# Performance work log

Hardware: AMD Instinct MI355X
Metric: run time of the kernel (lower is better)

## Reference

```python
import jax, jax.numpy as jnp
import numpy as np

N, NFEAT, NHID, NCLASS = 10000, 512, 256, 16
CRF_ITERS = 3


def setup_inputs() -> dict:
    key = jax.random.key(0)
    ks = jax.random.split(key, 10)
    x = jax.random.normal(ks[0], (N, NFEAT), dtype=jnp.float32)
    # sparse-ish adjacency: ~50 neighbors/node, self-loops, row-normalized (GCN style)
    mask = (jax.random.uniform(ks[1], (N, N)) < 0.005).astype(jnp.float32)
    adj = mask + jnp.eye(N, dtype=jnp.float32)
    adj = adj / jnp.sum(adj, axis=1, keepdims=True)
    s1 = 1.0 / np.sqrt(NFEAT)
    s2 = 1.0 / np.sqrt(NHID)
    W1 = jax.random.normal(ks[2], (NFEAT, NHID), dtype=jnp.float32) * s1
    b1 = jnp.zeros((NHID,), dtype=jnp.float32)
    Wq = jax.random.normal(ks[3], (NHID, NHID), dtype=jnp.float32) * s2
    Wk = jax.random.normal(ks[4], (NHID, NHID), dtype=jnp.float32) * s2
    alpha = jnp.float32(1.0)
    beta = jnp.float32(1.0)
    ln_w = jnp.ones((NHID,), dtype=jnp.float32)
    ln_b = jnp.zeros((NHID,), dtype=jnp.float32)
    W2 = jax.random.normal(ks[5], (NHID, NCLASS), dtype=jnp.float32) * s2
    b2 = jnp.zeros((NCLASS,), dtype=jnp.float32)
    return {"x": x, "adj": adj, "W1": W1, "b1": b1, "Wq": Wq, "Wk": Wk,
            "alpha": alpha, "beta": beta, "ln_w": ln_w, "ln_b": ln_b,
            "W2": W2, "b2": b2}


def reference(x, adj, W1, b1, Wq, Wk, alpha, beta, ln_w, ln_b, W2, b2):
    # gc1: adj @ (x W1) + b1, then relu
    h = jax.nn.relu(adj @ (x @ W1) + b1)          # [N, NHID]
    # CRF_Node: adjacency-masked similarity attention, 3 mean-field iterations
    q = h @ Wq
    k = h @ Wk
    scores = (q @ k.T) / jnp.sqrt(jnp.float32(NHID))  # [N, N]
    logits = jnp.where(adj > 0, scores, jnp.float32(-1e9))
    attn = jax.nn.softmax(logits, axis=-1)
    out = h
    for _ in range(CRF_ITERS):
        out = (alpha * h + beta * (attn @ out)) / (alpha + beta)
    # LayerNorm over feature dim
    mu = jnp.mean(out, axis=-1, keepdims=True)
    var = jnp.var(out, axis=-1, keepdims=True)
    out = (out - mu) * jax.lax.rsqrt(var + 1e-5) * ln_w + ln_b
    # dropout: eval mode (identity)
    # gc2 + log_softmax
    y = adj @ (out @ W2) + b2                     # [N, NCLASS]
    return jax.nn.log_softmax(y, axis=-1)
```

## Files before the change

kernel.cpp:

```cpp
#include <hip/hip_runtime.h>
#include <math.h>
#include <float.h>

#define N_NODES 10000
#define NFEAT   512
#define NHID    256
#define NCLASS  16
#define CAP     128

__device__ __forceinline__ float wave_sum(float v) {
#pragma unroll
  for (int o = 32; o > 0; o >>= 1) v += __shfl_down(v, o, 64);
  return v;
}
__device__ __forceinline__ float wave_max(float v) {
#pragma unroll
  for (int o = 32; o > 0; o >>= 1) v = fmaxf(v, __shfl_down(v, o, 64));
  return v;
}

__global__ __launch_bounds__(256) void gemm64(const float* __restrict__ A,
                                              const float* __restrict__ B,
                                              float* __restrict__ C,
                                              int M, int K, int N) {
  __shared__ float As[16][68];
  __shared__ float Bs[16][68];
  const int tid  = threadIdx.x;
  const int row0 = blockIdx.x * 64;
  const int col0 = blockIdx.y * 64;
  const int ty = tid >> 4, tx = tid & 15;
  const int arow = tid >> 2;
  const int akq  = (tid & 3) << 2;
  const int brow = tid >> 4;
  const int bcol = (tid & 15) << 2;

  float acc[4][4] = {};
  for (int k0 = 0; k0 < K; k0 += 16) {
    float4 av = make_float4(0.f, 0.f, 0.f, 0.f);
    const int gr = row0 + arow;
    if (gr < M) av = *(const float4*)&A[(size_t)gr * K + k0 + akq];
    As[akq + 0][arow] = av.x;
    As[akq + 1][arow] = av.y;
    As[akq + 2][arow] = av.z;
    As[akq + 3][arow] = av.w;
    const float4 bv = *(const float4*)&B[(size_t)(k0 + brow) * N + col0 + bcol];
    *(float4*)&Bs[brow][bcol] = bv;
    __syncthreads();
#pragma unroll
    for (int k = 0; k < 16; ++k) {
      const float4 a = *(const float4*)&As[k][ty << 2];
      const float4 b = *(const float4*)&Bs[k][tx << 2];
      acc[0][0] += a.x * b.x; acc[0][1] += a.x * b.y; acc[0][2] += a.x * b.z; acc[0][3] += a.x * b.w;
      acc[1][0] += a.y * b.x; acc[1][1] += a.y * b.y; acc[1][2] += a.y * b.z; acc[1][3] += a.y * b.w;
      acc[2][0] += a.z * b.x; acc[2][1] += a.z * b.y; acc[2][2] += a.z * b.z; acc[2][3] += a.z * b.w;
      acc[3][0] += a.w * b.x; acc[3][1] += a.w * b.y; acc[3][2] += a.w * b.z; acc[3][3] += a.w * b.w;
    }
    __syncthreads();
  }
#pragma unroll
  for (int j = 0; j < 4; ++j) {
    const int gr = row0 + (ty << 2) + j;
    if (gr < M) {
      const float4 o = make_float4(acc[j][0], acc[j][1], acc[j][2], acc[j][3]);
      *(float4*)&C[(size_t)gr * N + col0 + (tx << 2)] = o;
    }
  }
}

__global__ __launch_bounds__(256) void wqwkT(const float* __restrict__ Wq,
                                             const float* __restrict__ Wk,
                                             float* __restrict__ Mm) {
  __shared__ float qr[NHID];
  const int a = blockIdx.x, tid = threadIdx.x;
  qr[tid] = Wq[a * NHID + tid];
  __syncthreads();
  const float* kb = &Wk[(size_t)tid * NHID];
  float acc = 0.f;
#pragma unroll 8
  for (int c = 0; c < NHID; ++c) acc += qr[c] * kb[c];
  Mm[a * NHID + tid] = acc;
}

__global__ __launch_bounds__(256) void scan_build(const float* __restrict__ adj,
                                                  const float* __restrict__ xW1,
                                                  const float* __restrict__ b1,
                                                  int* __restrict__ cols,
                                                  float* __restrict__ vals,
                                                  int* __restrict__ nnz,
                                                  float* __restrict__ h) {
  __shared__ int   lcols[CAP];
  __shared__ float lvals[CAP];
  __shared__ int   scols[CAP];
  __shared__ float svals[CAP];
  __shared__ int   cnt;
  const int row = blockIdx.x, tid = threadIdx.x;
  if (tid == 0) cnt = 0;
  __syncthreads();
  const float4* arow = (const float4*)&adj[(size_t)row * N_NODES];
  for (int v = tid; v < N_NODES / 4; v += 256) {
    const float4 f = arow[v];
    if (f.x != 0.f) { int p = atomicAdd(&cnt, 1); if (p < CAP) { lcols[p] = 4 * v + 0; lvals[p] = f.x; } }
    if (f.y != 0.f) { int p = atomicAdd(&cnt, 1); if (p < CAP) { lcols[p] = 4 * v + 1; lvals[p] = f.y; } }
    if (f.z != 0.f) { int p = atomicAdd(&cnt, 1); if (p < CAP) { lcols[p] = 4 * v + 2; lvals[p] = f.z; } }
    if (f.w != 0.f) { int p = atomicAdd(&cnt, 1); if (p < CAP) { lcols[p] = 4 * v + 3; lvals[p] = f.w; } }
  }
  __syncthreads();
  const int c = min(cnt, CAP);
  int myc = 0; float myv = 0.f; int rank = 0;
  if (tid < c) {
    myc = lcols[tid]; myv = lvals[tid];
    for (int e = 0; e < c; ++e) rank += (lcols[e] < myc);
  }
  __syncthreads();
  if (tid < c) { scols[rank] = myc; svals[rank] = myv; }
  __syncthreads();
  if (tid == 0) nnz[row] = c;
  if (tid < c) {
    cols[(size_t)row * CAP + tid] = scols[tid];
    vals[(size_t)row * CAP + tid] = svals[tid];
  }
  float acc = b1[tid];
  for (int e = 0; e < c; ++e)
    acc += svals[e] * xW1[(size_t)scols[e] * NHID + tid];
  h[(size_t)row * NHID + tid] = fmaxf(acc, 0.f);
}

__global__ __launch_bounds__(256) void attn_crf1(const float* __restrict__ t,
                                                 const float* __restrict__ h,
                                                 const int* __restrict__ cols,
                                                 const int* __restrict__ nnz,
                                                 float* __restrict__ attn,
                                                 float* __restrict__ outn,
                                                 const float* __restrict__ alpha_p,
                                                 const float* __restrict__ beta_p) {
  __shared__ float s[CAP];
  __shared__ int   lcols[CAP];
  __shared__ float lv[CAP];
  __shared__ float red[4], red2[4];
  const int row = blockIdx.x, tid = threadIdx.x;
  const int lane = tid & 63, wv = tid >> 6;
  const int c = nnz[row];
  if (tid < c) lcols[tid] = cols[(size_t)row * CAP + tid];
  const float4 tq = *(const float4*)&t[(size_t)row * NHID + (lane << 2)];
  __syncthreads();
  for (int e = wv; e < c; e += 4) {
    const float4 kq = *(const float4*)&h[(size_t)lcols[e] * NHID + (lane << 2)];
    float p = tq.x * kq.x + tq.y * kq.y + tq.z * kq.z + tq.w * kq.w;
    p = wave_sum(p);
    if (lane == 0) s[e] = p * 0.0625f;
  }
  __syncthreads();
  float m = (tid < c) ? s[tid] : -FLT_MAX;
  m = wave_max(m);
  if (lane == 0) red[wv] = m;
  __syncthreads();
  m = fmaxf(fmaxf(red[0], red[1]), fmaxf(red[2], red[3]));
  const float ev = (tid < c) ? expf(s[tid] - m) : 0.f;
  float sum = wave_sum(ev);
  if (lane == 0) red2[wv] = sum;
  __syncthreads();
  sum = red2[0] + red2[1] + red2[2] + red2[3];
  if (tid < c) {
    const float a = ev / sum;
    attn[(size_t)row * CAP + tid] = a;
    lv[tid] = a;
  }
  __syncthreads();
  float acc = 0.f;
  for (int e = 0; e < c; ++e)
    acc += lv[e] * h[(size_t)lcols[e] * NHID + tid];
  const float a = alpha_p[0], b = beta_p[0];
  outn[(size_t)row * NHID + tid] =
      (a * h[(size_t)row * NHID + tid] + b * acc) / (a + b);
}

__global__ __launch_bounds__(256) void crf_iter(const float* __restrict__ h,
                                                const float* __restrict__ attn,
                                                const int* __restrict__ cols,
                                                const int* __restrict__ nnz,
                                                const float* __restrict__ outp,
                                                float* __restrict__ outn,
                                                const float* __restrict__ alpha_p,
                                                const float* __restrict__ beta_p) {
  __shared__ int   lcols[CAP];
  __shared__ float lv[CAP];
  const int row = blockIdx.x, tid = threadIdx.x;
  const int c = nnz[row];
  if (tid < c) {
    lcols[tid] = cols[(size_t)row * CAP + tid];
    lv[tid]    = attn[(size_t)row * CAP + tid];
  }
  __syncthreads();
  float acc = 0.f;
  for (int e = 0; e < c; ++e)
    acc += lv[e] * outp[(size_t)lcols[e] * NHID + tid];
  const float a = alpha_p[0], b = beta_p[0];
  outn[(size_t)row * NHID + tid] =
      (a * h[(size_t)row * NHID + tid] + b * acc) / (a + b);
}

__global__ __launch_bounds__(256) void crf_ln_w2(const float* __restrict__ h,
                                                 const float* __restrict__ attn,
                                                 const int* __restrict__ cols,
                                                 const int* __restrict__ nnz,
                                                 const float* __restrict__ outp,
                                                 const float* __restrict__ alpha_p,
                                                 const float* __restrict__ beta_p,
                                                 const float* __restrict__ lnw,
                                                 const float* __restrict__ lnb,
                                                 const float* __restrict__ W2,
                                                 float* __restrict__ z) {
  __shared__ int   lcols[CAP];
  __shared__ float lv[CAP];
  __shared__ float r1[4], r2[4], vs[NHID];
  __shared__ float part[16][17];
  const int row = blockIdx.x, tid = threadIdx.x;
  const int lane = tid & 63, wv = tid >> 6;
  const int c = nnz[row];
  if (tid < c) {
    lcols[tid] = cols[(size_t)row * CAP + tid];
    lv[tid]    = attn[(size_t)row * CAP + tid];
  }
  __syncthreads();
  float acc = 0.f;
  for (int e = 0; e < c; ++e)
    acc += lv[e] * outp[(size_t)lcols[e] * NHID + tid];
  const float a = alpha_p[0], b = beta_p[0];
  const float x = (a * h[(size_t)row * NHID + tid] + b * acc) / (a + b);
  float s = wave_sum(x);
  if (lane == 0) r1[wv] = s;
  __syncthreads();
  const float mu = (r1[0] + r1[1] + r1[2] + r1[3]) * (1.f / NHID);
  const float d = x - mu;
  float s2 = wave_sum(d * d);
  if (lane == 0) r2[wv] = s2;
  __syncthreads();
  const float var = (r2[0] + r2[1] + r2[2] + r2[3]) * (1.f / NHID);
  const float v = d * rsqrtf(var + 1e-5f) * lnw[tid] + lnb[tid];
  vs[tid] = v;
  __syncthreads();
  const int cc = tid & 15, g = tid >> 4;
  float p = 0.f;
#pragma unroll
  for (int u = 0; u < 16; ++u)
    p += vs[(g << 4) + u] * W2[((g << 4) + u) * NCLASS + cc];
  part[g][cc] = p;
  __syncthreads();
  if (tid < NCLASS) {
    float q = 0.f;
#pragma unroll
    for (int g2 = 0; g2 < 16; ++g2) q += part[g2][tid];
    z[(size_t)row * NCLASS + tid] = q;
  }
}

__global__ __launch_bounds__(256) void final_k(const float* __restrict__ z,
                                               const float* __restrict__ vals,
                                               const int* __restrict__ cols,
                                               const int* __restrict__ nnz,
                                               const float* __restrict__ b2,
                                               float* __restrict__ out) {
  __shared__ int   lcols[CAP];
  __shared__ float lv[CAP];
  __shared__ float part[16][17];
  __shared__ float ys[16];
  const int row = blockIdx.x, tid = threadIdx.x;
  const int c = nnz[row];
  if (tid < c) {
    lcols[tid] = cols[(size_t)row * CAP + tid];
    lv[tid]    = vals[(size_t)row * CAP + tid];
  }
  __syncthreads();
  const int cc = tid & 15, g = tid >> 4;
  float acc = 0.f;
  for (int e = g; e < c; e += 16)
    acc += lv[e] * z[(size_t)lcols[e] * NCLASS + cc];
  part[g][cc] = acc;
  __syncthreads();
  if (tid < NCLASS) {
    float y = b2[tid];
#pragma unroll
    for (int g2 = 0; g2 < 16; ++g2) y += part[g2][tid];
    ys[tid] = y;
  }
  __syncthreads();
  if (tid < NCLASS) {
    float m = ys[0];
#pragma unroll
    for (int i = 1; i < 16; ++i) m = fmaxf(m, ys[i]);
    float ssum = 0.f;
#pragma unroll
    for (int i = 0; i < 16; ++i) ssum += expf(ys[i] - m);
    out[(size_t)row * NCLASS + tid] = ys[tid] - m - logf(ssum);
  }
}

extern "C" void kernel_launch(void* const* d_in, const int* in_sizes, int n_in,
                              void* d_out, int out_size, void* d_ws, size_t ws_size,
                              hipStream_t stream) {
  const float* x   = (const float*)d_in[0];
  const float* adj = (const float*)d_in[1];
  const float* W1  = (const float*)d_in[2];
  const float* b1  = (const float*)d_in[3];
  const float* Wq  = (const float*)d_in[4];
  const float* Wk  = (const float*)d_in[5];
  const float* al  = (const float*)d_in[6];
  const float* be  = (const float*)d_in[7];
  const float* lnw = (const float*)d_in[8];
  const float* lnb = (const float*)d_in[9];
  const float* W2  = (const float*)d_in[10];
  const float* b2  = (const float*)d_in[11];
  float* out = (float*)d_out;

  char* w = (char*)d_ws;
  size_t off = 0;
  auto alloc = [&](size_t bytes) -> void* {
    void* p = (void*)(w + off);
    off += (bytes + 255) & ~(size_t)255;
    return p;
  };
  float* bufA = (float*)alloc(sizeof(float) * N_NODES * NHID);
  float* h    = (float*)alloc(sizeof(float) * N_NODES * NHID);
  float* outA = (float*)alloc(sizeof(float) * N_NODES * NHID);
  float* Mm   = (float*)alloc(sizeof(float) * NHID * NHID);
  float* z    = (float*)alloc(sizeof(float) * N_NODES * NCLASS);
  int*   cols = (int*)  alloc(sizeof(int)   * N_NODES * CAP);
  float* vals = (float*)alloc(sizeof(float) * N_NODES * CAP);
  float* attn = (float*)alloc(sizeof(float) * N_NODES * CAP);
  int*   nnz  = (int*)  alloc(sizeof(int)   * N_NODES);
  float* xW1  = bufA;
  float* t    = bufA;
  float* outB = bufA;

  const dim3 gg((N_NODES + 63) / 64, NHID / 64);

  gemm64<<<gg, 256, 0, stream>>>(x, W1, xW1, N_NODES, NFEAT, NHID);
  wqwkT<<<NHID, 256, 0, stream>>>(Wq, Wk, Mm);
  scan_build<<<N_NODES, 256, 0, stream>>>(adj, xW1, b1, cols, vals, nnz, h);
  gemm64<<<gg, 256, 0, stream>>>(h, Mm, t, N_NODES, NHID, NHID);
  attn_crf1<<<N_NODES, 256, 0, stream>>>(t, h, cols, nnz, attn, outA, al, be);
  crf_iter<<<N_NODES, 256, 0, stream>>>(h, attn, cols, nnz, outA, outB, al, be);
  crf_ln_w2<<<N_NODES, 256, 0, stream>>>(h, attn, cols, nnz, outB, al, be,
                                         lnw, lnb, W2, z);
  final_k<<<N_NODES, 256, 0, stream>>>(z, vals, cols, nnz, b2, out);
}
```

Baseline: 877.8 us.

## Map one wavefront per row with float4 gathers across sparse CRF kernels

```diff
diff --git a/kernel.cpp b/kernel.cpp
--- a/kernel.cpp
+++ b/kernel.cpp
@@ -8,16 +8,7 @@
 #define NCLASS  16
 #define CAP     128
 
-__device__ __forceinline__ float wave_sum(float v) {
-#pragma unroll
-  for (int o = 32; o > 0; o >>= 1) v += __shfl_down(v, o, 64);
-  return v;
-}
-__device__ __forceinline__ float wave_max(float v) {
-#pragma unroll
-  for (int o = 32; o > 0; o >>= 1) v = fmaxf(v, __shfl_down(v, o, 64));
-  return v;
-}
+typedef float nfloat4 __attribute__((ext_vector_type(4)));
 
 __global__ __launch_bounds__(256) void gemm64(const float* __restrict__ A,
                                               const float* __restrict__ B,
@@ -70,15 +61,19 @@
 __global__ __launch_bounds__(256) void wqwkT(const float* __restrict__ Wq,
                                              const float* __restrict__ Wk,
                                              float* __restrict__ Mm) {
-  __shared__ float qr[NHID];
+  __shared__ float4 qr4[NHID / 4];
   const int a = blockIdx.x, tid = threadIdx.x;
-  qr[tid] = Wq[a * NHID + tid];
-  __syncthreads();
-  const float* kb = &Wk[(size_t)tid * NHID];
+  if (tid < NHID / 4) qr4[tid] = ((const float4*)&Wq[(size_t)a * NHID])[tid];
+  __syncthreads();
+  const float4* kb = (const float4*)&Wk[(size_t)tid * NHID];
   float acc = 0.f;
 #pragma unroll 8
-  for (int c = 0; c < NHID; ++c) acc += qr[c] * kb[c];
-  Mm[a * NHID + tid] = acc;
+  for (int c4 = 0; c4 < NHID / 4; ++c4) {
+    const float4 k4 = kb[c4];
+    const float4 q4 = qr4[c4];
+    acc += q4.x * k4.x + q4.y * k4.y + q4.z * k4.z + q4.w * k4.w;
+  }
+  Mm[(size_t)a * NHID + tid] = acc;
 }
 
 __global__ __launch_bounds__(256) void scan_build(const float* __restrict__ adj,
@@ -88,17 +83,18 @@
                                                   float* __restrict__ vals,
                                                   int* __restrict__ nnz,
                                                   float* __restrict__ h) {
-  __shared__ int   lcols[CAP];
-  __shared__ float lvals[CAP];
-  __shared__ int   scols[CAP];
-  __shared__ float svals[CAP];
-  __shared__ int   cnt;
+  __shared__ int    lcols[CAP];
+  __shared__ float  lvals[CAP];
+  __shared__ int    scols[CAP];
+  __shared__ float  svals[CAP];
+  __shared__ float4 pacc[4][64];
+  __shared__ int    cnt;
   const int row = blockIdx.x, tid = threadIdx.x;
   if (tid == 0) cnt = 0;
   __syncthreads();
-  const float4* arow = (const float4*)&adj[(size_t)row * N_NODES];
+  const nfloat4* arow = (const nfloat4*)&adj[(size_t)row * N_NODES];
   for (int v = tid; v < N_NODES / 4; v += 256) {
-    const float4 f = arow[v];
+    const nfloat4 f = __builtin_nontemporal_load(&arow[v]);
     if (f.x != 0.f) { int p = atomicAdd(&cnt, 1); if (p < CAP) { lcols[p] = 4 * v + 0; lvals[p] = f.x; } }
     if (f.y != 0.f) { int p = atomicAdd(&cnt, 1); if (p < CAP) { lcols[p] = 4 * v + 1; lvals[p] = f.y; } }
     if (f.z != 0.f) { int p = atomicAdd(&cnt, 1); if (p < CAP) { lcols[p] = 4 * v + 2; lvals[p] = f.z; } }
@@ -119,10 +115,26 @@
     cols[(size_t)row * CAP + tid] = scols[tid];
     vals[(size_t)row * CAP + tid] = svals[tid];
   }
-  float acc = b1[tid];
-  for (int e = 0; e < c; ++e)
-    acc += svals[e] * xW1[(size_t)scols[e] * NHID + tid];
-  h[(size_t)row * NHID + tid] = fmaxf(acc, 0.f);
+  const int lane = tid & 63, wv = tid >> 6;
+  float4 acc = make_float4(0.f, 0.f, 0.f, 0.f);
+  for (int e = wv; e < c; e += 4) {
+    const float vv = svals[e];
+    const float4 xv = *(const float4*)&xW1[(size_t)scols[e] * NHID + (lane << 2)];
+    acc.x += vv * xv.x; acc.y += vv * xv.y; acc.z += vv * xv.z; acc.w += vv * xv.w;
+  }
+  pacc[wv][lane] = acc;
+  __syncthreads();
+  if (wv == 0) {
+    const float4 p0 = pacc[0][lane], p1 = pacc[1][lane];
+    const float4 p2 = pacc[2][lane], p3 = pacc[3][lane];
+    const float4 bb = *(const float4*)&b1[lane << 2];
+    float4 r;
+    r.x = fmaxf(bb.x + ((p0.x + p1.x) + (p2.x + p3.x)), 0.f);
+    r.y = fmaxf(bb.y + ((p0.y + p1.y) + (p2.y + p3.y)), 0.f);
+    r.z = fmaxf(bb.z + ((p0.z + p1.z) + (p2.z + p3.z)), 0.f);
+    r.w = fmaxf(bb.w + ((p0.w + p1.w) + (p2.w + p3.w)), 0.f);
+    *(float4*)&h[(size_t)row * NHID + (lane << 2)] = r;
+  }
 }
 
 __global__ __launch_bounds__(256) void attn_crf1(const float* __restrict__ t,
@@ -133,45 +145,70 @@
                                                  float* __restrict__ outn,
                                                  const float* __restrict__ alpha_p,
                                                  const float* __restrict__ beta_p) {
-  __shared__ float s[CAP];
-  __shared__ int   lcols[CAP];
-  __shared__ float lv[CAP];
-  __shared__ float red[4], red2[4];
-  const int row = blockIdx.x, tid = threadIdx.x;
-  const int lane = tid & 63, wv = tid >> 6;
+  __shared__ int   lcols[4][CAP];
+  __shared__ float sv[4][CAP];
+  const int tid = threadIdx.x, lane = tid & 63, wv = tid >> 6;
+  const int row = (blockIdx.x << 2) + wv;
   const int c = nnz[row];
-  if (tid < c) lcols[tid] = cols[(size_t)row * CAP + tid];
-  const float4 tq = *(const float4*)&t[(size_t)row * NHID + (lane << 2)];
-  __syncthreads();
-  for (int e = wv; e < c; e += 4) {
-    const float4 kq = *(const float4*)&h[(size_t)lcols[e] * NHID + (lane << 2)];
-    float p = tq.x * kq.x + tq.y * kq.y + tq.z * kq.z + tq.w * kq.w;
-    p = wave_sum(p);
-    if (lane == 0) s[e] = p * 0.0625f;
-  }
-  __syncthreads();
-  float m = (tid < c) ? s[tid] : -FLT_MAX;
-  m = wave_max(m);
-  if (lane == 0) red[wv] = m;
-  __syncthreads();
-  m = fmaxf(fmaxf(red[0], red[1]), fmaxf(red[2], red[3]));
-  const float ev = (tid < c) ? expf(s[tid] - m) : 0.f;
-  float sum = wave_sum(ev);
-  if (lane == 0) red2[wv] = sum;
-  __syncthreads();
-  sum = red2[0] + red2[1] + red2[2] + red2[3];
-  if (tid < c) {
-    const float a = ev / sum;
-    attn[(size_t)row * CAP + tid] = a;
-    lv[tid] = a;
-  }
-  __syncthreads();
-  float acc = 0.f;
-  for (int e = 0; e < c; ++e)
-    acc += lv[e] * h[(size_t)lcols[e] * NHID + tid];
+  for (int e = lane; e < c; e += 64) lcols[wv][e] = cols[(size_t)row * CAP + e];
+  const int gq = lane >> 4, gl = lane & 15;
+  const float* tp = &t[(size_t)row * NHID + (gl << 2)];
+  const float4 t0 = *(const float4*)&tp[0];
+  const float4 t1 = *(const float4*)&tp[64];
+  const float4 t2 = *(const float4*)&tp[128];
+  const float4 t3 = *(const float4*)&tp[192];
+  for (int e = gq; e < c; e += 4) {
+    const float* hp = &h[(size_t)lcols[wv][e] * NHID + (gl << 2)];
+    const float4 h0 = *(const float4*)&hp[0];
+    const float4 h1 = *(const float4*)&hp[64];
+    const float4 h2 = *(const float4*)&hp[128];
+    const float4 h3 = *(const float4*)&hp[192];
+    float p = t0.x * h0.x + t0.y * h0.y + t0.z * h0.z + t0.w * h0.w
+            + t1.x * h1.x + t1.y * h1.y + t1.z * h1.z + t1.w * h1.w
+            + t2.x * h2.x + t2.y * h2.y + t2.z * h2.z + t2.w * h2.w
+            + t3.x * h3.x + t3.y * h3.y + t3.z * h3.z + t3.w * h3.w;
+    p += __shfl_xor(p, 1, 64);
+    p += __shfl_xor(p, 2, 64);
+    p += __shfl_xor(p, 4, 64);
+    p += __shfl_xor(p, 8, 64);
+    if (gl == 0) sv[wv][e] = p * 0.0625f;
+  }
+  const float s1 = (lane      < c) ? sv[wv][lane]      : -FLT_MAX;
+  const float s2 = (lane + 64 < c) ? sv[wv][lane + 64] : -FLT_MAX;
+  float m = fmaxf(s1, s2);
+#pragma unroll
+  for (int o = 32; o > 0; o >>= 1) m = fmaxf(m, __shfl_xor(m, o, 64));
+  const float e1 = (lane      < c) ? __expf(s1 - m) : 0.f;
+  const float e2 = (lane + 64 < c) ? __expf(s2 - m) : 0.f;
+  float sum = e1 + e2;
+#pragma unroll
+  for (int o = 32; o > 0; o >>= 1) sum += __shfl_xor(sum, o, 64);
+  const float inv = 1.f / sum;
+  if (lane < c) {
+    const float aw = e1 * inv;
+    sv[wv][lane] = aw;
+    attn[(size_t)row * CAP + lane] = aw;
+  }
+  if (lane + 64 < c) {
+    const float aw = e2 * inv;
+    sv[wv][lane + 64] = aw;
+    attn[(size_t)row * CAP + lane + 64] = aw;
+  }
+  float4 acc = make_float4(0.f, 0.f, 0.f, 0.f);
+  for (int e = 0; e < c; ++e) {
+    const float ve = sv[wv][e];
+    const float4 xv = *(const float4*)&h[(size_t)lcols[wv][e] * NHID + (lane << 2)];
+    acc.x += ve * xv.x; acc.y += ve * xv.y; acc.z += ve * xv.z; acc.w += ve * xv.w;
+  }
   const float a = alpha_p[0], b = beta_p[0];
-  outn[(size_t)row * NHID + tid] =
-      (a * h[(size_t)row * NHID + tid] + b * acc) / (a + b);
+  const float i2 = 1.f / (a + b);
+  const float4 hq = *(const float4*)&h[(size_t)row * NHID + (lane << 2)];
+  float4 o4;
+  o4.x = (a * hq.x + b * acc.x) * i2;
+  o4.y = (a * hq.y + b * acc.y) * i2;
+  o4.z = (a * hq.z + b * acc.z) * i2;
+  o4.w = (a * hq.w + b * acc.w) * i2;
+  *(float4*)&outn[(size_t)row * NHID + (lane << 2)] = o4;
 }
 
 __global__ __launch_bounds__(256) void crf_iter(const float* __restrict__ h,
@@ -182,21 +219,39 @@
                                                 float* __restrict__ outn,
                                                 const float* __restrict__ alpha_p,
                                                 const float* __restrict__ beta_p) {
-  __shared__ int   lcols[CAP];
-  __shared__ float lv[CAP];
-  const int row = blockIdx.x, tid = threadIdx.x;
+  __shared__ int   lcols[4][CAP];
+  __shared__ float lv[4][CAP];
+  const int tid = threadIdx.x, lane = tid & 63, wv = tid >> 6;
+  const int row = (blockIdx.x << 2) + wv;
   const int c = nnz[row];
-  if (tid < c) {
-    lcols[tid] = cols[(size_t)row * CAP + tid];
-    lv[tid]    = attn[(size_t)row * CAP + tid];
-  }
-  __syncthreads();
-  float acc = 0.f;
-  for (int e = 0; e < c; ++e)
-    acc += lv[e] * outp[(size_t)lcols[e] * NHID + tid];
+  for (int e = lane; e < c; e += 64) {
+    lcols[wv][e] = cols[(size_t)row * CAP + e];
+    lv[wv][e]   = attn[(size_t)row * CAP + e];
+  }
+  float4 acc = make_float4(0.f, 0.f, 0.f, 0.f);
+  int e = 0;
+  for (; e + 1 < c; e += 2) {
+    const int   c0 = lcols[wv][e],   c1 = lcols[wv][e + 1];
+    const float v0 = lv[wv][e],      v1 = lv[wv][e + 1];
+    const float4 x0 = *(const float4*)&outp[(size_t)c0 * NHID + (lane << 2)];
+    const float4 x1 = *(const float4*)&outp[(size_t)c1 * NHID + (lane << 2)];
+    acc.x += v0 * x0.x; acc.y += v0 * x0.y; acc.z += v0 * x0.z; acc.w += v0 * x0.w;
+    acc.x += v1 * x1.x; acc.y += v1 * x1.y; acc.z += v1 * x1.z; acc.w += v1 * x1.w;
+  }
+  if (e < c) {
+    const float ve = lv[wv][e];
+    const float4 xv = *(const float4*)&outp[(size_t)lcols[wv][e] * NHID + (lane << 2)];
+    acc.x += ve * xv.x; acc.y += ve * xv.y; acc.z += ve * xv.z; acc.w += ve * xv.w;
+  }
   const float a = alpha_p[0], b = beta_p[0];
-  outn[(size_t)row * NHID + tid] =
-      (a * h[(size_t)row * NHID + tid] + b * acc) / (a + b);
+  const float i2 = 1.f / (a + b);
+  const float4 hq = *(const float4*)&h[(size_t)row * NHID + (lane << 2)];
+  float4 o4;
+  o4.x = (a * hq.x + b * acc.x) * i2;
+  o4.y = (a * hq.y + b * acc.y) * i2;
+  o4.z = (a * hq.z + b * acc.z) * i2;
+  o4.w = (a * hq.w + b * acc.w) * i2;
+  *(float4*)&outn[(size_t)row * NHID + (lane << 2)] = o4;
 }
 
 __global__ __launch_bounds__(256) void crf_ln_w2(const float* __restrict__ h,
@@ -210,47 +265,67 @@
                                                  const float* __restrict__ lnb,
                                                  const float* __restrict__ W2,
                                                  float* __restrict__ z) {
-  __shared__ int   lcols[CAP];
-  __shared__ float lv[CAP];
-  __shared__ float r1[4], r2[4], vs[NHID];
+  __shared__ int   lcols[4][CAP];
+  __shared__ float lv[4][CAP];
+  __shared__ float vs[4][NHID];
   __shared__ float part[16][17];
-  const int row = blockIdx.x, tid = threadIdx.x;
-  const int lane = tid & 63, wv = tid >> 6;
+  const int tid = threadIdx.x, lane = tid & 63, wv = tid >> 6;
+  const int row = (blockIdx.x << 2) + wv;
   const int c = nnz[row];
-  if (tid < c) {
-    lcols[tid] = cols[(size_t)row * CAP + tid];
-    lv[tid]    = attn[(size_t)row * CAP + tid];
-  }
-  __syncthreads();
-  float acc = 0.f;
-  for (int e = 0; e < c; ++e)
-    acc += lv[e] * outp[(size_t)lcols[e] * NHID + tid];
+  for (int e = lane; e < c; e += 64) {
+    lcols[wv][e] = cols[(size_t)row * CAP + e];
+    lv[wv][e]   = attn[(size_t)row * CAP + e];
+  }
+  float4 acc = make_float4(0.f, 0.f, 0.f, 0.f);
+  for (int e = 0; e < c; ++e) {
+    const float ve = lv[wv][e];
+    const float4 xv = *(const float4*)&outp[(size_t)lcols[wv][e] * NHID + (lane << 2)];
+    acc.x += ve * xv.x; acc.y += ve * xv.y; acc.z += ve * xv.z; acc.w += ve * xv.w;
+  }
   const float a = alpha_p[0], b = beta_p[0];
-  const float x = (a * h[(size_t)row * NHID + tid] + b * acc) / (a + b);
-  float s = wave_sum(x);
-  if (lane == 0) r1[wv] = s;
-  __syncthreads();
-  const float mu = (r1[0] + r1[1] + r1[2] + r1[3]) * (1.f / NHID);
-  const float d = x - mu;
-  float s2 = wave_sum(d * d);
-  if (lane == 0) r2[wv] = s2;
-  __syncthreads();
-  const float var = (r2[0] + r2[1] + r2[2] + r2[3]) * (1.f / NHID);
-  const float v = d * rsqrtf(var + 1e-5f) * lnw[tid] + lnb[tid];
-  vs[tid] = v;
-  __syncthreads();
-  const int cc = tid & 15, g = tid >> 4;
-  float p = 0.f;
-#pragma unroll
-  for (int u = 0; u < 16; ++u)
-    p += vs[(g << 4) + u] * W2[((g << 4) + u) * NCLASS + cc];
-  part[g][cc] = p;
-  __syncthreads();
-  if (tid < NCLASS) {
-    float q = 0.f;
-#pragma unroll
-    for (int g2 = 0; g2 < 16; ++g2) q += part[g2][tid];
-    z[(size_t)row * NCLASS + tid] = q;
+  const float i2 = 1.f / (a + b);
+  const float4 hq = *(const float4*)&h[(size_t)row * NHID + (lane << 2)];
+  float4 x4;
+  x4.x = (a * hq.x + b * acc.x) * i2;
+  x4.y = (a * hq.y + b * acc.y) * i2;
+  x4.z = (a * hq.z + b * acc.z) * i2;
+  x4.w = (a * hq.w + b * acc.w) * i2;
+  float s = x4.x + x4.y + x4.z + x4.w;
+#pragma unroll
+  for (int o = 32; o > 0; o >>= 1) s += __shfl_xor(s, o, 64);
+  const float mu = s * (1.f / NHID);
+  float4 d4;
+  d4.x = x4.x - mu; d4.y = x4.y - mu; d4.z = x4.z - mu; d4.w = x4.w - mu;
+  float v = d4.x * d4.x + d4.y * d4.y + d4.z * d4.z + d4.w * d4.w;
+#pragma unroll
+  for (int o = 32; o > 0; o >>= 1) v += __shfl_xor(v, o, 64);
+  const float rstd = rsqrtf(v * (1.f / NHID) + 1e-5f);
+  const float4 lw = *(const float4*)&lnw[lane << 2];
+  const float4 lb = *(const float4*)&lnb[lane << 2];
+  float4 v4;
+  v4.x = d4.x * rstd * lw.x + lb.x;
+  v4.y = d4.y * rstd * lw.y + lb.y;
+  v4.z = d4.z * rstd * lw.z + lb.z;
+  v4.w = d4.w * rstd * lw.w + lb.w;
+  *(float4*)&vs[wv][lane << 2] = v4;
+  __syncthreads();
+  const int g = tid >> 4, cc = tid & 15;
+  float w2f[16];
+#pragma unroll
+  for (int u = 0; u < 16; ++u) w2f[u] = W2[(size_t)((g << 4) + u) * NCLASS + cc];
+  for (int rr = 0; rr < 4; ++rr) {
+    float p = 0.f;
+#pragma unroll
+    for (int u = 0; u < 16; ++u) p += vs[rr][(g << 4) + u] * w2f[u];
+    part[g][cc] = p;
+    __syncthreads();
+    if (tid < NCLASS) {
+      float q = 0.f;
+#pragma unroll
+      for (int g2 = 0; g2 < 16; ++g2) q += part[g2][tid];
+      z[(size_t)((blockIdx.x << 2) + rr) * NCLASS + tid] = q;
+    }
+    __syncthreads();
   }
 }
 
@@ -260,39 +335,30 @@
                                                const int* __restrict__ nnz,
                                                const float* __restrict__ b2,
                                                float* __restrict__ out) {
-  __shared__ int   lcols[CAP];
-  __shared__ float lv[CAP];
-  __shared__ float part[16][17];
-  __shared__ float ys[16];
-  const int row = blockIdx.x, tid = threadIdx.x;
+  __shared__ int   lcols[4][CAP];
+  __shared__ float lv[4][CAP];
+  const int tid = threadIdx.x, lane = tid & 63, wv = tid >> 6;
+  const int row = (blockIdx.x << 2) + wv;
   const int c = nnz[row];
-  if (tid < c) {
-    lcols[tid] = cols[(size_t)row * CAP + tid];
-    lv[tid]    = vals[(size_t)row * CAP + tid];
-  }
-  __syncthreads();
-  const int cc = tid & 15, g = tid >> 4;
+  for (int e = lane; e < c; e += 64) {
+    lcols[wv][e] = cols[(size_t)row * CAP + e];
+    lv[wv][e]   = vals[(size_t)row * CAP + e];
+  }
+  const int eg = lane >> 4, cc = lane & 15;
   float acc = 0.f;
-  for (int e = g; e < c; e += 16)
-    acc += lv[e] * z[(size_t)lcols[e] * NCLASS + cc];
-  part[g][cc] = acc;
-  __syncthreads();
-  if (tid < NCLASS) {
-    float y = b2[tid];
-#pragma unroll
-    for (int g2 = 0; g2 < 16; ++g2) y += part[g2][tid];
-    ys[tid] = y;
-  }
-  __syncthreads();
-  if (tid < NCLASS) {
-    float m = ys[0];
-#pragma unroll
-    for (int i = 1; i < 16; ++i) m = fmaxf(m, ys[i]);
-    float ssum = 0.f;
-#pragma unroll
-    for (int i = 0; i < 16; ++i) ssum += expf(ys[i] - m);
-    out[(size_t)row * NCLASS + tid] = ys[tid] - m - logf(ssum);
-  }
+  for (int e = eg; e < c; e += 4)
+    acc += lv[wv][e] * z[(size_t)lcols[wv][e] * NCLASS + cc];
+  acc += __shfl_xor(acc, 16, 64);
+  acc += __shfl_xor(acc, 32, 64);
+  const float y = acc + b2[cc];
+  float m = y;
+#pragma unroll
+  for (int o = 8; o > 0; o >>= 1) m = fmaxf(m, __shfl_xor(m, o, 64));
+  const float ev = __expf(y - m);
+  float sme = ev;
+#pragma unroll
+  for (int o = 8; o > 0; o >>= 1) sme += __shfl_xor(sme, o, 64);
+  if (eg == 0) out[(size_t)row * NCLASS + cc] = y - m - logf(sme);
 }
 
 extern "C" void kernel_launch(void* const* d_in, const int* in_sizes, int n_in,
@@ -333,14 +399,15 @@
   float* outB = bufA;
 
   const dim3 gg((N_NODES + 63) / 64, NHID / 64);
+  const int rb = N_NODES / 4;
 
   gemm64<<<gg, 256, 0, stream>>>(x, W1, xW1, N_NODES, NFEAT, NHID);
   wqwkT<<<NHID, 256, 0, stream>>>(Wq, Wk, Mm);
   scan_build<<<N_NODES, 256, 0, stream>>>(adj, xW1, b1, cols, vals, nnz, h);
   gemm64<<<gg, 256, 0, stream>>>(h, Mm, t, N_NODES, NHID, NHID);
-  attn_crf1<<<N_NODES, 256, 0, stream>>>(t, h, cols, nnz, attn, outA, al, be);
-  crf_iter<<<N_NODES, 256, 0, stream>>>(h, attn, cols, nnz, outA, outB, al, be);
-  crf_ln_w2<<<N_NODES, 256, 0, stream>>>(h, attn, cols, nnz, outB, al, be,
-                                         lnw, lnb, W2, z);
-  final_k<<<N_NODES, 256, 0, stream>>>(z, vals, cols, nnz, b2, out);
-}
+  attn_crf1<<<rb, 256, 0, stream>>>(t, h, cols, nnz, attn, outA, al, be);
+  crf_iter<<<rb, 256, 0, stream>>>(h, attn, cols, nnz, outA, outB, al, be);
+  crf_ln_w2<<<rb, 256, 0, stream>>>(h, attn, cols, nnz, outB, al, be,
+                                    lnw, lnb, W2, z);
+  final_k<<<rb, 256, 0, stream>>>(z, vals, cols, nnz, b2, out);
+}
```

After: 840.2 us. -4.3%, faster.
